# Performance work log

Measured on AMD Instinct MI355X. Metric: run time of the kernel, lower is better.

## Reference

```python
import jax, jax.numpy as jnp
import numpy as np

N_NODES = 50000


def rgcn_conv(x, src, dst, edge_type, W, root, bias):
    """PyG RGCNConv: out[i] = x[i] @ root + bias + sum_r mean_{j in N_r(i)} x[j] @ W[r].
    W: [R, F_in, F_out]. Mean aggregation is per-relation (PyG default aggr='mean')."""
    num_rel = W.shape[0]
    n = x.shape[0]
    out = x @ root + bias
    x_src = x[src]  # [E, F_in] gather once
    for r in range(num_rel):  # small fixed relation count
        mask = (edge_type == r)
        msg = jnp.where(mask[:, None], x_src, 0.0) @ W[r]          # [E, F_out]
        s = jax.ops.segment_sum(msg, dst, num_segments=n)           # [N, F_out]
        c = jax.ops.segment_sum(mask.astype(x.dtype), dst, num_segments=n)  # [N]
        out = out + s / jnp.maximum(c, 1.0)[:, None]
    return out


def setup_inputs() -> dict:
    key = jax.random.key(0)
    ks = jax.random.split(key, 10)
    N, E, F_in, F_hid, F_out, R = N_NODES, 800000, 128, 128, 64, 8
    x = jax.random.normal(ks[0], (N, F_in), dtype=jnp.float32)
    edge_index = jax.random.randint(ks[1], (2, E), 0, N, dtype=jnp.int64)
    edge_type = jax.random.randint(ks[2], (E,), 0, R, dtype=jnp.int64)
    s1 = 1.0 / np.sqrt(F_in)
    s2 = 1.0 / np.sqrt(F_hid)
    W1 = jax.random.normal(ks[3], (R, F_in, F_hid), dtype=jnp.float32) * s1
    root1 = jax.random.normal(ks[4], (F_in, F_hid), dtype=jnp.float32) * s1
    b1 = jnp.zeros((F_hid,), dtype=jnp.float32)
    W2 = jax.random.normal(ks[5], (R, F_hid, F_out), dtype=jnp.float32) * s2
    root2 = jax.random.normal(ks[6], (F_hid, F_out), dtype=jnp.float32) * s2
    b2 = jnp.zeros((F_out,), dtype=jnp.float32)
    return {"x": x, "edge_index": edge_index, "edge_type": edge_type,
            "W1": W1, "root1": root1, "b1": b1,
            "W2": W2, "root2": root2, "b2": b2}


def reference(x, edge_index, edge_type, W1, root1, b1, W2, root2, b2):
    src, dst = edge_index[0], edge_index[1]
    h = jax.nn.relu(rgcn_conv(x, src, dst, edge_type, W1, root1, b1))
    out = rgcn_conv(h, src, dst, edge_type, W2, root2, b2)
    return out
```

## Files before the change

kernel.cpp:

```cpp
#include <hip/hip_runtime.h>

#define N_NODES 50000
#define N_EDGES 800000
#define R_REL   8
#define NR      (N_NODES * R_REL)
#define SCAN_CHUNK 2048
#define SCAN_NBLK  ((NR + SCAN_CHUNK - 1) / SCAN_CHUNK)

#define NBKT    196
#define BNSH    8
#define BKEYS   2048
#define BCAP    5120
#define SLAB    2048
#define BINBLK  ((N_EDGES + SLAB - 1) / SLAB)

typedef float  f32x4  __attribute__((ext_vector_type(4)));
typedef __bf16 bf16x8 __attribute__((ext_vector_type(8)));

__device__ __forceinline__ unsigned short f2bf(float f) {
    unsigned int u = __float_as_uint(f);
    u = (u + 0x7FFFu + ((u >> 16) & 1u)) >> 16;
    return (unsigned short)u;
}
__device__ __forceinline__ float bflo(unsigned int u) { return __uint_as_float(u << 16); }
__device__ __forceinline__ float bfhi(unsigned int u) { return __uint_as_float(u & 0xFFFF0000u); }

__device__ __forceinline__ void acc16(float* a, uint4 u0, uint4 u1) {
    a[0]  += bflo(u0.x);   a[1]  += bfhi(u0.x);
    a[2]  += bflo(u0.y);   a[3]  += bfhi(u0.y);
    a[4]  += bflo(u0.z);   a[5]  += bfhi(u0.z);
    a[6]  += bflo(u0.w);   a[7]  += bfhi(u0.w);
    a[8]  += bflo(u1.x);   a[9]  += bfhi(u1.x);
    a[10] += bflo(u1.y);   a[11] += bfhi(u1.y);
    a[12] += bflo(u1.z);   a[13] += bfhi(u1.z);
    a[14] += bflo(u1.w);   a[15] += bfhi(u1.w);
}


__global__ __launch_bounds__(256) void k_binA(
    const int* __restrict__ src, const int* __restrict__ dst,
    const int* __restrict__ et, int* __restrict__ gcur,
    uint2* __restrict__ gbin)
{
    __shared__ int hist[NBKT];
    __shared__ int base[NBKT];
    const int t = threadIdx.x;
    const int e0 = blockIdx.x * SLAB;
    for (int i = t; i < NBKT; i += 256) hist[i] = 0;
    __syncthreads();
#pragma unroll
    for (int i = 0; i < SLAB / 256; ++i) {
        int e = e0 + i * 256 + t;
        if (e < N_EDGES) atomicAdd(&hist[dst[e] >> BNSH], 1);
    }
    __syncthreads();
    for (int i = t; i < NBKT; i += 256) {
        int h = hist[i];
        base[i] = (h > 0) ? atomicAdd(&gcur[i], h) : 0;
        hist[i] = 0;
    }
    __syncthreads();
#pragma unroll
    for (int i = 0; i < SLAB / 256; ++i) {
        int e = e0 + i * 256 + t;
        if (e < N_EDGES) {
            int d = dst[e];
            int b = d >> BNSH;
            int sub = atomicAdd(&hist[b], 1);
            gbin[b * BCAP + base[b] + sub] =
                make_uint2((unsigned)src[e], (unsigned)(d * 8 + et[e]));
        }
    }
}

__global__ __launch_bounds__(256) void k_bcount(
    const int* __restrict__ gcur, const uint2* __restrict__ gbin,
    int* __restrict__ cnt)
{
    __shared__ int lc[BKEYS];
    const int t = threadIdx.x;
    const int b = blockIdx.x;
    for (int i = t; i < BKEYS; i += 256) lc[i] = 0;
    __syncthreads();
    const int n = gcur[b];
    const uint2* rec = gbin + (size_t)b * BCAP;
    const int kbase = b * BKEYS;
    for (int j = t; j < n; j += 256)
        atomicAdd(&lc[rec[j].y - kbase], 1);
    __syncthreads();
    for (int i = t; i < BKEYS; i += 256) {
        int k = kbase + i;
        if (k < NR) cnt[k] = lc[i];
    }
}

__global__ __launch_bounds__(256) void k_bscat(
    const int* __restrict__ gcur, const uint2* __restrict__ gbin,
    const int* __restrict__ offs, int* __restrict__ srcS)
{
    __shared__ int cur[BKEYS];
    const int t = threadIdx.x;
    const int b = blockIdx.x;
    for (int i = t; i < BKEYS; i += 256) cur[i] = 0;
    __syncthreads();
    const int n = gcur[b];
    const uint2* rec = gbin + (size_t)b * BCAP;
    const int kbase = b * BKEYS;
    for (int j = t; j < n; j += 256) {
        uint2 r = rec[j];
        int sub = atomicAdd(&cur[r.y - kbase], 1);
        srcS[offs[r.y] + sub] = (int)r.x;
    }
}


__global__ void k_scan1(const int* __restrict__ cnt, int* __restrict__ offs,
                        int* __restrict__ bsum) {
    __shared__ int sd[256];
    int t = threadIdx.x;
    int base = blockIdx.x * SCAN_CHUNK + t * 8;
    int v[8];
    int tot = 0;
#pragma unroll
    for (int i = 0; i < 8; i++) {
        int idx = base + i;
        int xv = (idx < NR) ? cnt[idx] : 0;
        v[i] = tot;
        tot += xv;
    }
    sd[t] = tot;
    __syncthreads();
    for (int off = 1; off < 256; off <<= 1) {
        int y = (t >= off) ? sd[t - off] : 0;
        __syncthreads();
        sd[t] += y;
        __syncthreads();
    }
    int excl = sd[t] - tot;
#pragma unroll
    for (int i = 0; i < 8; i++) {
        int idx = base + i;
        if (idx < NR) offs[idx] = v[i] + excl;
    }
    if (t == 255) bsum[blockIdx.x] = sd[255];
}

__global__ void k_scan2(const int* __restrict__ bsum, int* __restrict__ bsum2) {
    __shared__ int sd[256];
    int t = threadIdx.x;
    int v = (t < SCAN_NBLK) ? bsum[t] : 0;
    sd[t] = v;
    __syncthreads();
    for (int off = 1; off < 256; off <<= 1) {
        int y = (t >= off) ? sd[t - off] : 0;
        __syncthreads();
        sd[t] += y;
        __syncthreads();
    }
    bsum2[t] = sd[t] - v;
}

__global__ void k_scan3(int* __restrict__ offs, const int* __restrict__ bsum2) {
    int t = threadIdx.x;
    int b = blockIdx.x;
    int add = bsum2[b];
    int base = b * SCAN_CHUNK + t * 8;
#pragma unroll
    for (int i = 0; i < 8; i++) {
        int idx = base + i;
        if (idx < NR) offs[idx] += add;
    }
    if (b == 0 && t == 0) offs[NR] = N_EDGES;
}


__global__ void k_cvt_x(const float* __restrict__ x, unsigned short* __restrict__ xb, int n4) {
    int i = blockIdx.x * 256 + threadIdx.x;
    if (i < n4) {
        float4 v = *(const float4*)(x + (size_t)i * 4);
        ushort4 o;
        o.x = f2bf(v.x); o.y = f2bf(v.y); o.z = f2bf(v.z); o.w = f2bf(v.w);
        *(ushort4*)(xb + (size_t)i * 4) = o;
    }
}

#define W1_ELEMS (9 * 128 * 128)
#define W2_ELEMS (9 * 64 * 128)
__global__ void k_wprep_all(const float* __restrict__ root1, const float* __restrict__ W1,
                            const float* __restrict__ root2, const float* __restrict__ W2,
                            unsigned short* __restrict__ Wt1, unsigned short* __restrict__ Wt2) {
    int idx = blockIdx.x * 256 + threadIdx.x;
    if (idx < W1_ELEMS) {
        int j    = idx & 7;
        int lane = (idx >> 3) & 63;
        int r    = idx >> 9;
        int nb   = r & 7;
        int r2   = r >> 3;
        int kk   = r2 & 3;
        int seg  = r2 >> 2;
        int k = kk * 32 + (lane >> 4) * 8 + j;
        int n = nb * 16 + (lane & 15);
        float v = (seg == 0) ? root1[k * 128 + n] : W1[((seg - 1) * 128 + k) * 128 + n];
        Wt1[idx] = f2bf(v);
    } else if (idx < W1_ELEMS + W2_ELEMS) {
        int i2   = idx - W1_ELEMS;
        int j    = i2 & 7;
        int lane = (i2 >> 3) & 63;
        int r    = i2 >> 9;
        int nb   = r & 3;
        int r2   = r >> 2;
        int kk   = r2 & 3;
        int seg  = r2 >> 2;
        int k = kk * 32 + (lane >> 4) * 8 + j;
        int n = nb * 16 + (lane & 15);
        float v = (seg == 0) ? root2[k * 64 + n] : W2[((seg - 1) * 128 + k) * 64 + n];
        Wt2[i2] = f2bf(v);
    }
}


template <int FOUT, bool RELU, bool OUT_BF16>
__global__ __launch_bounds__(512) void k_fused(
    const unsigned short* __restrict__ xin,
    const unsigned short* __restrict__ WtP,
    const float* __restrict__ bias,
    const int* __restrict__ offs,
    const int* __restrict__ srcS,
    unsigned short* __restrict__ outb,
    float* __restrict__ outf)
{
    constexpr int NBt = FOUT / 16;
    __shared__ __align__(16) unsigned short As[9][16][136];

    const int t = threadIdx.x;
    const int node0 = blockIdx.x * 16;

    if (t < 128) {
        const int sr = t >> 3;
        const int sp = t & 7;
        const uint4* src = (const uint4*)(xin + (size_t)(node0 + sr) * 128 + sp * 16);
        uint4 r0 = src[0], r1 = src[1];
        uint4* d = (uint4*)&As[0][sr][sp * 16];
        d[0] = r0; d[1] = r1;
    }

    {
        const int nl  = t >> 5;
        const int rel = (t >> 2) & 7;
        const int q   = t & 3;

        const int pair = (node0 + nl) * 8 + rel;
        const int beg = offs[pair];
        const int end = offs[pair + 1];
        const int deg = end - beg;

        const unsigned short* bx = xin + q * 32;
        float a[32];
#pragma unroll
        for (int i = 0; i < 32; ++i) a[i] = 0.f;

        int j = beg;
        for (; j + 1 < end; j += 2) {
            int s0 = srcS[j];
            int s1 = srcS[j + 1];
            const uint4* p0 = (const uint4*)(bx + (size_t)s0 * 128);
            const uint4* p1 = (const uint4*)(bx + (size_t)s1 * 128);
            uint4 v0 = p0[0], v1 = p0[1], v2 = p0[2], v3 = p0[3];
            uint4 w0 = p1[0], w1 = p1[1], w2 = p1[2], w3 = p1[3];
            acc16(a, v0, v1);
            acc16(a + 16, v2, v3);
            acc16(a, w0, w1);
            acc16(a + 16, w2, w3);
        }
        if (j < end) {
            int s = srcS[j];
            const uint4* p = (const uint4*)(bx + (size_t)s * 128);
            uint4 v0 = p[0], v1 = p[1], v2 = p[2], v3 = p[3];
            acc16(a, v0, v1);
            acc16(a + 16, v2, v3);
        }

        float scl = 1.f / (float)(deg > 1 ? deg : 1);
        unsigned int pk[16];
#pragma unroll
        for (int i = 0; i < 16; ++i)
            pk[i] = (unsigned int)f2bf(a[i * 2] * scl) |
                    ((unsigned int)f2bf(a[i * 2 + 1] * scl) << 16);
        uint4* d = (uint4*)&As[1 + rel][nl][q * 32];
        d[0] = make_uint4(pk[0],  pk[1],  pk[2],  pk[3]);
        d[1] = make_uint4(pk[4],  pk[5],  pk[6],  pk[7]);
        d[2] = make_uint4(pk[8],  pk[9],  pk[10], pk[11]);
        d[3] = make_uint4(pk[12], pk[13], pk[14], pk[15]);
    }

    __syncthreads();

    const int lane = t & 63;
    const int w = t >> 6;
    if (w >= NBt) return;
    const int quad = lane >> 4;
    const int tc = lane & 15;

    f32x4 acc = (f32x4){0.f, 0.f, 0.f, 0.f};
    const bf16x8* Bp = (const bf16x8*)WtP;

#pragma unroll
    for (int seg = 0; seg < 9; ++seg) {
        const unsigned short* Arow = &As[seg][tc][0];
#pragma unroll
        for (int kk = 0; kk < 4; ++kk) {
            bf16x8 af = *(const bf16x8*)(Arow + kk * 32 + quad * 8);
            bf16x8 bf = Bp[((seg * 4 + kk) * NBt + w) * 64 + lane];
            acc = __builtin_amdgcn_mfma_f32_16x16x32_bf16(af, bf, acc, 0, 0, 0);
        }
    }

    const int col = w * 16 + tc;
    const float bs = bias[col];
#pragma unroll
    for (int i = 0; i < 4; ++i) {
        int r = node0 + quad * 4 + i;
        float v = acc[i] + bs;
        if (RELU) v = fmaxf(v, 0.f);
        if (OUT_BF16) outb[(size_t)r * FOUT + col] = f2bf(v);
        else          outf[(size_t)r * FOUT + col] = v;
    }
}


extern "C" void kernel_launch(void* const* d_in, const int* in_sizes, int n_in,
                              void* d_out, int out_size, void* d_ws, size_t ws_size,
                              hipStream_t stream) {
    const float* x     = (const float*)d_in[0];
    const int*   ei    = (const int*)d_in[1];
    const int*   et    = (const int*)d_in[2];
    const float* W1    = (const float*)d_in[3];
    const float* root1 = (const float*)d_in[4];
    const float* b1    = (const float*)d_in[5];
    const float* W2    = (const float*)d_in[6];
    const float* root2 = (const float*)d_in[7];
    const float* b2    = (const float*)d_in[8];
    float* out = (float*)d_out;

    int* ws     = (int*)d_ws;
    int* cnt    = ws;
    int* offs   = cnt + NR;
    int* wt2buf = offs + NR + 128;
    int* bsum   = wt2buf + NR;
    int* bsum2  = bsum + 256;
    int* gcur   = bsum2 + 256;
    int* srcS   = gcur + 256;
    unsigned short* xb  = (unsigned short*)(srcS + N_EDGES);
    unsigned short* hb  = xb + (size_t)N_NODES * 128;
    uint2* gbin = (uint2*)(hb + (size_t)N_NODES * 128);
    unsigned short* Wt1 = (unsigned short*)cnt;
    unsigned short* Wt2 = (unsigned short*)wt2buf;

    hipMemsetAsync(gcur, 0, 256 * sizeof(int), stream);
    k_binA<<<BINBLK, 256, 0, stream>>>(ei, ei + N_EDGES, et, gcur, gbin);
    k_bcount<<<NBKT, 256, 0, stream>>>(gcur, gbin, cnt);
    k_scan1<<<SCAN_NBLK, 256, 0, stream>>>(cnt, offs, bsum);
    k_scan2<<<1, 256, 0, stream>>>(bsum, bsum2);
    k_scan3<<<SCAN_NBLK, 256, 0, stream>>>(offs, bsum2);
    k_bscat<<<NBKT, 256, 0, stream>>>(gcur, gbin, offs, srcS);

    k_wprep_all<<<(W1_ELEMS + W2_ELEMS + 255) / 256, 256, 0, stream>>>(
        root1, W1, root2, W2, Wt1, Wt2);
    k_cvt_x<<<(N_NODES * 32 + 255) / 256, 256, 0, stream>>>(x, xb, N_NODES * 32);

    const int NT = N_NODES / 16;

    k_fused<128, true,  true ><<<NT, 512, 0, stream>>>(xb, Wt1, b1, offs, srcS, hb, nullptr);
    k_fused<64,  false, false><<<NT, 512, 0, stream>>>(hb, Wt2, b2, offs, srcS, nullptr, out);
}
```

Baseline: 261.3 us.

## Fuse preprocessing kernels, split gather across 1024 threads, swizzle LDS tiles

Merges the CSR build into fewer launches. Bucket counting now does the per-bucket scan, and the final scatter also does the bucket-sum scan and applies the offsets, replacing the separate scan kernels. The x conversion, weight packing and gcur reset are combined into one kernel. The fused RGCN kernel moves to 1024 threads, with each thread gathering 16 features over a 4-edge unrolled loop, and uses an XOR swizzle on the LDS tile to reduce bank conflicts. This cuts launch overhead and raises gather parallelism, at the cost of higher register pressure from launch_bounds(1024,4).

```diff
diff --git a/kernel.cpp b/kernel.cpp
--- a/kernel.cpp
+++ b/kernel.cpp
@@ -4,8 +4,6 @@
 #define N_EDGES 800000
 #define R_REL   8
 #define NR      (N_NODES * R_REL)
-#define SCAN_CHUNK 2048
-#define SCAN_NBLK  ((NR + SCAN_CHUNK - 1) / SCAN_CHUNK)
 
 #define NBKT    196
 #define BNSH    8
@@ -73,11 +71,12 @@
     }
 }
 
-__global__ __launch_bounds__(256) void k_bcount(
+__global__ __launch_bounds__(256) void k_bcount_scan(
     const int* __restrict__ gcur, const uint2* __restrict__ gbin,
-    int* __restrict__ cnt)
+    int* __restrict__ offs, int* __restrict__ bsum)
 {
     __shared__ int lc[BKEYS];
+    __shared__ int sd[256];
     const int t = threadIdx.x;
     const int b = blockIdx.x;
     for (int i = t; i < BKEYS; i += 256) lc[i] = 0;
@@ -88,43 +87,12 @@
     for (int j = t; j < n; j += 256)
         atomicAdd(&lc[rec[j].y - kbase], 1);
     __syncthreads();
-    for (int i = t; i < BKEYS; i += 256) {
-        int k = kbase + i;
-        if (k < NR) cnt[k] = lc[i];
-    }
-}
-
-__global__ __launch_bounds__(256) void k_bscat(
-    const int* __restrict__ gcur, const uint2* __restrict__ gbin,
-    const int* __restrict__ offs, int* __restrict__ srcS)
-{
-    __shared__ int cur[BKEYS];
-    const int t = threadIdx.x;
-    const int b = blockIdx.x;
-    for (int i = t; i < BKEYS; i += 256) cur[i] = 0;
-    __syncthreads();
-    const int n = gcur[b];
-    const uint2* rec = gbin + (size_t)b * BCAP;
-    const int kbase = b * BKEYS;
-    for (int j = t; j < n; j += 256) {
-        uint2 r = rec[j];
-        int sub = atomicAdd(&cur[r.y - kbase], 1);
-        srcS[offs[r.y] + sub] = (int)r.x;
-    }
-}
-
-
-__global__ void k_scan1(const int* __restrict__ cnt, int* __restrict__ offs,
-                        int* __restrict__ bsum) {
-    __shared__ int sd[256];
-    int t = threadIdx.x;
-    int base = blockIdx.x * SCAN_CHUNK + t * 8;
+    const int base = t * 8;
     int v[8];
     int tot = 0;
 #pragma unroll
     for (int i = 0; i < 8; i++) {
-        int idx = base + i;
-        int xv = (idx < NR) ? cnt[idx] : 0;
+        int xv = lc[base + i];
         v[i] = tot;
         tot += xv;
     }
@@ -139,16 +107,25 @@
     int excl = sd[t] - tot;
 #pragma unroll
     for (int i = 0; i < 8; i++) {
-        int idx = base + i;
-        if (idx < NR) offs[idx] = v[i] + excl;
-    }
-    if (t == 255) bsum[blockIdx.x] = sd[255];
-}
-
-__global__ void k_scan2(const int* __restrict__ bsum, int* __restrict__ bsum2) {
+        int k = kbase + base + i;
+        if (k < NR) offs[k] = v[i] + excl;
+    }
+    if (t == 255) bsum[b] = sd[255];
+}
+
+__global__ __launch_bounds__(256) void k_bscat_final(
+    const int* __restrict__ gcur, const uint2* __restrict__ gbin,
+    const int* __restrict__ bsum, int* __restrict__ offs,
+    int* __restrict__ srcS)
+{
+    __shared__ int obase[BKEYS];
+    __shared__ int cur[BKEYS];
     __shared__ int sd[256];
-    int t = threadIdx.x;
-    int v = (t < SCAN_NBLK) ? bsum[t] : 0;
+    __shared__ int sadd;
+    const int t = threadIdx.x;
+    const int b = blockIdx.x;
+
+    int v = (t < NBKT) ? bsum[t] : 0;
     sd[t] = v;
     __syncthreads();
     for (int off = 1; off < 256; off <<= 1) {
@@ -157,39 +134,51 @@
         sd[t] += y;
         __syncthreads();
     }
-    bsum2[t] = sd[t] - v;
-}
-
-__global__ void k_scan3(int* __restrict__ offs, const int* __restrict__ bsum2) {
-    int t = threadIdx.x;
-    int b = blockIdx.x;
-    int add = bsum2[b];
-    int base = b * SCAN_CHUNK + t * 8;
-#pragma unroll
-    for (int i = 0; i < 8; i++) {
-        int idx = base + i;
-        if (idx < NR) offs[idx] += add;
+    if (t == b) sadd = sd[t] - v;
+    __syncthreads();
+    const int add = sadd;
+
+    const int kbase = b * BKEYS;
+    for (int i = t; i < BKEYS; i += 256) {
+        int k = kbase + i;
+        int o = ((k < NR) ? offs[k] : 0) + add;
+        obase[i] = o;
+        cur[i] = 0;
+        if (k < NR) offs[k] = o;
     }
     if (b == 0 && t == 0) offs[NR] = N_EDGES;
-}
-
-
-__global__ void k_cvt_x(const float* __restrict__ x, unsigned short* __restrict__ xb, int n4) {
-    int i = blockIdx.x * 256 + threadIdx.x;
-    if (i < n4) {
-        float4 v = *(const float4*)(x + (size_t)i * 4);
+    __syncthreads();
+
+    const int n = gcur[b];
+    const uint2* rec = gbin + (size_t)b * BCAP;
+    for (int j = t; j < n; j += 256) {
+        uint2 r = rec[j];
+        int li = r.y - kbase;
+        int sub = atomicAdd(&cur[li], 1);
+        srcS[obase[li] + sub] = (int)r.x;
+    }
+}
+
+
+#define W1_ELEMS (9 * 128 * 128)
+#define W2_ELEMS (9 * 64 * 128)
+#define N4       (N_NODES * 32)
+
+__global__ __launch_bounds__(256) void k_cvtw(
+    const float* __restrict__ x, unsigned short* __restrict__ xb,
+    const float* __restrict__ root1, const float* __restrict__ W1,
+    const float* __restrict__ root2, const float* __restrict__ W2,
+    unsigned short* __restrict__ Wt1, unsigned short* __restrict__ Wt2,
+    int* __restrict__ gcur)
+{
+    const int idx = blockIdx.x * 256 + threadIdx.x;
+    if (blockIdx.x == 0) gcur[threadIdx.x] = 0;
+    if (idx < N4) {
+        float4 v = *(const float4*)(x + (size_t)idx * 4);
         ushort4 o;
         o.x = f2bf(v.x); o.y = f2bf(v.y); o.z = f2bf(v.z); o.w = f2bf(v.w);
-        *(ushort4*)(xb + (size_t)i * 4) = o;
-    }
-}
-
-#define W1_ELEMS (9 * 128 * 128)
-#define W2_ELEMS (9 * 64 * 128)
-__global__ void k_wprep_all(const float* __restrict__ root1, const float* __restrict__ W1,
-                            const float* __restrict__ root2, const float* __restrict__ W2,
-                            unsigned short* __restrict__ Wt1, unsigned short* __restrict__ Wt2) {
-    int idx = blockIdx.x * 256 + threadIdx.x;
+        *(ushort4*)(xb + (size_t)idx * 4) = o;
+    }
     if (idx < W1_ELEMS) {
         int j    = idx & 7;
         int lane = (idx >> 3) & 63;
@@ -220,7 +209,7 @@
 
 
 template <int FOUT, bool RELU, bool OUT_BF16>
-__global__ __launch_bounds__(512) void k_fused(
+__global__ __launch_bounds__(1024, 4) void k_fused(
     const unsigned short* __restrict__ xin,
     const unsigned short* __restrict__ WtP,
     const float* __restrict__ bias,
@@ -245,52 +234,63 @@
     }
 
     {
-        const int nl  = t >> 5;
-        const int rel = (t >> 2) & 7;
-        const int q   = t & 3;
+        const int oct = t & 7;
+        const int rel = (t >> 3) & 7;
+        const int nl  = t >> 6;
 
         const int pair = (node0 + nl) * 8 + rel;
         const int beg = offs[pair];
         const int end = offs[pair + 1];
         const int deg = end - beg;
 
-        const unsigned short* bx = xin + q * 32;
-        float a[32];
-#pragma unroll
-        for (int i = 0; i < 32; ++i) a[i] = 0.f;
+        const unsigned short* bx = xin + oct * 16;
+        float a[16];
+#pragma unroll
+        for (int i = 0; i < 16; ++i) a[i] = 0.f;
 
         int j = beg;
-        for (; j + 1 < end; j += 2) {
-            int s0 = srcS[j];
-            int s1 = srcS[j + 1];
+        for (; j + 3 < end; j += 4) {
+            int s0 = srcS[j], s1 = srcS[j + 1], s2 = srcS[j + 2], s3 = srcS[j + 3];
             const uint4* p0 = (const uint4*)(bx + (size_t)s0 * 128);
             const uint4* p1 = (const uint4*)(bx + (size_t)s1 * 128);
-            uint4 v0 = p0[0], v1 = p0[1], v2 = p0[2], v3 = p0[3];
-            uint4 w0 = p1[0], w1 = p1[1], w2 = p1[2], w3 = p1[3];
-            acc16(a, v0, v1);
-            acc16(a + 16, v2, v3);
-            acc16(a, w0, w1);
-            acc16(a + 16, w2, w3);
+            const uint4* p2 = (const uint4*)(bx + (size_t)s2 * 128);
+            const uint4* p3 = (const uint4*)(bx + (size_t)s3 * 128);
+            uint4 u0 = p0[0], u1 = p0[1];
+            uint4 u2 = p1[0], u3 = p1[1];
+            uint4 u4 = p2[0], u5 = p2[1];
+            uint4 u6 = p3[0], u7 = p3[1];
+            acc16(a, u0, u1);
+            acc16(a, u2, u3);
+            acc16(a, u4, u5);
+            acc16(a, u6, u7);
+        }
+        if (j + 1 < end) {
+            int s0 = srcS[j], s1 = srcS[j + 1];
+            const uint4* p0 = (const uint4*)(bx + (size_t)s0 * 128);
+            const uint4* p1 = (const uint4*)(bx + (size_t)s1 * 128);
+            uint4 u0 = p0[0], u1 = p0[1];
+            uint4 u2 = p1[0], u3 = p1[1];
+            acc16(a, u0, u1);
+            acc16(a, u2, u3);
+            j += 2;
         }
         if (j < end) {
-            int s = srcS[j];
-            const uint4* p = (const uint4*)(bx + (size_t)s * 128);
-            uint4 v0 = p[0], v1 = p[1], v2 = p[2], v3 = p[3];
-            acc16(a, v0, v1);
-            acc16(a + 16, v2, v3);
+            int s0 = srcS[j];
+            const uint4* p0 = (const uint4*)(bx + (size_t)s0 * 128);
+            uint4 u0 = p0[0], u1 = p0[1];
+            acc16(a, u0, u1);
         }
 
         float scl = 1.f / (float)(deg > 1 ? deg : 1);
-        unsigned int pk[16];
-#pragma unroll
-        for (int i = 0; i < 16; ++i)
+        unsigned int pk[8];
+#pragma unroll
+        for (int i = 0; i < 8; ++i)
             pk[i] = (unsigned int)f2bf(a[i * 2] * scl) |
                     ((unsigned int)f2bf(a[i * 2 + 1] * scl) << 16);
-        uint4* d = (uint4*)&As[1 + rel][nl][q * 32];
-        d[0] = make_uint4(pk[0],  pk[1],  pk[2],  pk[3]);
-        d[1] = make_uint4(pk[4],  pk[5],  pk[6],  pk[7]);
-        d[2] = make_uint4(pk[8],  pk[9],  pk[10], pk[11]);
-        d[3] = make_uint4(pk[12], pk[13], pk[14], pk[15]);
+        uint4* G = (uint4*)&As[1 + rel][nl][0];
+        const int g0 = oct * 2;
+        G[g0 ^ rel]       = make_uint4(pk[0], pk[1], pk[2], pk[3]);
+        G[(g0 + 1) ^ rel] = make_uint4(pk[4], pk[5], pk[6], pk[7]);
     }
 
     __syncthreads();
@@ -306,10 +306,11 @@
 
 #pragma unroll
     for (int seg = 0; seg < 9; ++seg) {
-        const unsigned short* Arow = &As[seg][tc][0];
+        const uint4* Ag = (const uint4*)&As[seg][tc][0];
+        const int s = (seg == 0) ? 0 : (seg - 1);
 #pragma unroll
         for (int kk = 0; kk < 4; ++kk) {
-            bf16x8 af = *(const bf16x8*)(Arow + kk * 32 + quad * 8);
+            bf16x8 af = *(const bf16x8*)(Ag + (((kk << 2) + quad) ^ s));
             bf16x8 bf = Bp[((seg * 4 + kk) * NBt + w) * 64 + lane];
             acc = __builtin_amdgcn_mfma_f32_16x16x32_bf16(af, bf, acc, 0, 0, 0);
         }
@@ -356,20 +357,14 @@
     unsigned short* Wt1 = (unsigned short*)cnt;
     unsigned short* Wt2 = (unsigned short*)wt2buf;
 
-    hipMemsetAsync(gcur, 0, 256 * sizeof(int), stream);
+    k_cvtw<<<(N4 + 255) / 256, 256, 0, stream>>>(x, xb, root1, W1, root2, W2,
+                                                 Wt1, Wt2, gcur);
     k_binA<<<BINBLK, 256, 0, stream>>>(ei, ei + N_EDGES, et, gcur, gbin);
-    k_bcount<<<NBKT, 256, 0, stream>>>(gcur, gbin, cnt);
-    k_scan1<<<SCAN_NBLK, 256, 0, stream>>>(cnt, offs, bsum);
-    k_scan2<<<1, 256, 0, stream>>>(bsum, bsum2);
-    k_scan3<<<SCAN_NBLK, 256, 0, stream>>>(offs, bsum2);
-    k_bscat<<<NBKT, 256, 0, stream>>>(gcur, gbin, offs, srcS);
-
-    k_wprep_all<<<(W1_ELEMS + W2_ELEMS + 255) / 256, 256, 0, stream>>>(
-        root1, W1, root2, W2, Wt1, Wt2);
-    k_cvt_x<<<(N_NODES * 32 + 255) / 256, 256, 0, stream>>>(x, xb, N_NODES * 32);
+    k_bcount_scan<<<NBKT, 256, 0, stream>>>(gcur, gbin, offs, bsum);
+    k_bscat_final<<<NBKT, 256, 0, stream>>>(gcur, gbin, bsum, offs, srcS);
 
     const int NT = N_NODES / 16;
 
-    k_fused<128, true,  true ><<<NT, 512, 0, stream>>>(xb, Wt1, b1, offs, srcS, hb, nullptr);
-    k_fused<64,  false, false><<<NT, 512, 0, stream>>>(hb, Wt2, b2, offs, srcS, nullptr, out);
-}
+    k_fused<128, true,  true ><<<NT, 1024, 0, stream>>>(xb, Wt1, b1, offs, srcS, hb, nullptr);
+    k_fused<64,  false, false><<<NT, 1024, 0, stream>>>(hb, Wt2, b2, offs, srcS, nullptr, out);
+}
```

Measured after the change: 288.3 us. 10.3% more time.
